# Optimization experiments

Measured on AMD Instinct MI355X. Metric: run time of the kernel, lower is better.

## Reference

```python
import jax, jax.numpy as jnp
import numpy as np

T, D, I, E, G, LG, K = 2048, 1024, 512, 32, 8, 4, 6
SI = 2 * I  # shared expert inter dim = n_shared_experts * inter_dim
ROUTE_SCALE = 1.0


def setup_inputs() -> dict:
    key = jax.random.key(0)
    ks = jax.random.split(key, 16)
    s = 0.02
    f = jnp.float32
    return {
        "x": jax.random.normal(ks[0], (T, D), f),
        "router_w": jax.random.normal(ks[1], (E, D), f) * s,
        "router_b": jax.random.normal(ks[2], (E,), f) * s,
        "W1": jax.random.normal(ks[3], (E, D, I), f) * s,
        "b1": jax.random.normal(ks[4], (E, I), f) * s,
        "W2": jax.random.normal(ks[5], (E, D, I), f) * s,
        "b2": jax.random.normal(ks[6], (E, I), f) * s,
        "W3": jax.random.normal(ks[7], (E, I, D), f) * s,
        "b3": jax.random.normal(ks[8], (E, D), f) * s,
        "sw1": jax.random.normal(ks[9], (D, SI), f) * s,
        "sb1": jax.random.normal(ks[10], (SI,), f) * s,
        "sw2": jax.random.normal(ks[11], (D, SI), f) * s,
        "sb2": jax.random.normal(ks[12], (SI,), f) * s,
        "sw3": jax.random.normal(ks[13], (SI, D), f) * s,
        "sb3": jax.random.normal(ks[14], (D,), f) * s,
    }


def _route(x, router_w, router_b):
    # Router: softmax scores (fp32), group-limited top-k.
    logits = x @ router_w.T + router_b                      # [T, E]
    scores = jax.nn.softmax(logits.astype(jnp.float32), axis=-1)
    original = scores
    sg = scores.reshape(x.shape[0], G, E // G)              # [T, G, E/G]
    # no router bias -> group score = sum of top-2 expert scores per group
    group_scores = jnp.sum(jax.lax.top_k(sg, 2)[0], axis=-1)  # [T, G]
    _, gidx = jax.lax.top_k(group_scores, LG)               # [T, LG]
    keep = jnp.zeros((x.shape[0], G), bool).at[jnp.arange(x.shape[0])[:, None], gidx].set(True)
    masked = jnp.where(keep[:, :, None], sg, -jnp.inf).reshape(x.shape[0], E)
    _, idx = jax.lax.top_k(masked, K)                       # [T, K]
    vals = jnp.take_along_axis(original, idx, axis=1) * ROUTE_SCALE
    return vals.astype(x.dtype), idx


def reference(x, router_w, router_b, W1, b1, W2, b2, W3, b3, sw1, sb1, sw2, sb2, sw3, sb3):
    vals, idx = _route(x, router_w, router_b)
    # dense gate matrix [T, E]; top-k indices per row are distinct
    gates = jnp.zeros((x.shape[0], E), x.dtype).at[jnp.arange(x.shape[0])[:, None], idx].set(vals)
    # routed experts: Expert(x) = W3 @ silu(w1(x) * w2(x))
    h1 = jnp.einsum('td,edi->tei', x, W1) + b1              # [T, E, I]
    h2 = jnp.einsum('td,edi->tei', x, W2) + b2
    h = jax.nn.silu(h1 * h2)
    y = jnp.einsum('tei,eid->td', h * gates[:, :, None], W3) + gates @ b3
    # shared expert
    z = jax.nn.silu((x @ sw1 + sb1) * (x @ sw2 + sb2)) @ sw3 + sb3
    return y + z
```

## Files before the change

kernel.cpp:

```cpp
#include <hip/hip_runtime.h>
#include <hip/hip_bf16.h>
#include <math.h>

#define T_CONST 2048
#define D_CONST 1024
#define I_CONST 512
#define SI_CONST 1024
#define E_CONST 32
#define G_CONST 8
#define LG_CONST 4
#define KSEL 6
#define BK 32

typedef __attribute__((ext_vector_type(8))) short short8;
typedef __attribute__((ext_vector_type(4))) float floatx4;

__device__ inline unsigned pack_bf16(float a, float b) {
  __hip_bfloat162 h = __float22bfloat162_rn(float2{a, b});
  return *reinterpret_cast<unsigned*>(&h);
}

__device__ inline void gload16(const void* g, void* l) {
  __builtin_amdgcn_global_load_lds(
      (const __attribute__((address_space(1))) unsigned int*)g,
      (__attribute__((address_space(3))) unsigned int*)l, 16, 0, 0);
}

__global__ __launch_bounds__(256) void cvt_x(const float* __restrict__ in,
                                             __hip_bfloat16* __restrict__ out) {
  size_t i = ((size_t)blockIdx.x * 256 + threadIdx.x) * 4;
  float4 v = *(const float4*)&in[i];
  uint2 u{pack_bf16(v.x, v.y), pack_bf16(v.z, v.w)};
  *(uint2*)&out[i] = u;
}

__global__ __launch_bounds__(256) void cvt_rwt(const float* __restrict__ rw,
                                               float* __restrict__ rwt) {
  int i = blockIdx.x * 256 + threadIdx.x;
  int d = i >> 5, e = i & 31;
  rwt[d * 32 + e] = rw[e * D_CONST + d];
}

__global__ __launch_bounds__(256) void transpose_all(
    const float* __restrict__ W1, const float* __restrict__ W2,
    const float* __restrict__ W3, const float* __restrict__ sw1,
    const float* __restrict__ sw2, const float* __restrict__ sw3,
    __hip_bfloat16* __restrict__ W1t, __hip_bfloat16* __restrict__ W2t,
    __hip_bfloat16* __restrict__ W3t, __hip_bfloat16* __restrict__ sw1t,
    __hip_bfloat16* __restrict__ sw2t, __hip_bfloat16* __restrict__ sw3t) {
  __shared__ float tile[64][65];
  int b = blockIdx.x;
  const float* in;
  __hip_bfloat16* out;
  int K, N, k0, n0;
  if (b < 8192) {
    int local = b & 4095;
    int mat = local >> 7, rem = local & 127;
    K = 1024; N = 512;
    in = ((b < 4096) ? W1 : W2) + (size_t)mat * (1024 * 512);
    out = ((b < 4096) ? W1t : W2t) + (size_t)mat * (1024 * 512);
    n0 = (rem & 7) * 64; k0 = (rem >> 3) * 64;
  } else if (b < 12288) {
    int local = b - 8192;
    int mat = local >> 7, rem = local & 127;
    K = 512; N = 1024;
    in = W3 + (size_t)mat * (512 * 1024);
    out = W3t + (size_t)mat * (512 * 1024);
    n0 = (rem & 15) * 64; k0 = (rem >> 4) * 64;
  } else {
    int local = b - 12288;
    int which = local >> 8, rem = local & 255;
    K = 1024; N = 1024;
    in = which == 0 ? sw1 : which == 1 ? sw2 : sw3;
    out = which == 0 ? sw1t : which == 1 ? sw2t : sw3t;
    n0 = (rem & 15) * 64; k0 = (rem >> 4) * 64;
  }
  int tid = threadIdx.x;
  int tr = tid >> 4, tc4 = (tid & 15) * 4;
#pragma unroll
  for (int i = 0; i < 4; ++i) {
    float4 v = *(const float4*)&in[(size_t)(k0 + tr + 16 * i) * N + n0 + tc4];
    tile[tr + 16 * i][tc4 + 0] = v.x;
    tile[tr + 16 * i][tc4 + 1] = v.y;
    tile[tr + 16 * i][tc4 + 2] = v.z;
    tile[tr + 16 * i][tc4 + 3] = v.w;
  }
  __syncthreads();
#pragma unroll
  for (int i = 0; i < 4; ++i) {
    int n = tr + 16 * i;
    unsigned lo = pack_bf16(tile[tc4 + 0][n], tile[tc4 + 1][n]);
    unsigned hi = pack_bf16(tile[tc4 + 2][n], tile[tc4 + 3][n]);
    uint2 u{lo, hi};
    *(uint2*)&out[(size_t)(n0 + n) * K + k0 + tc4] = u;
  }
}

__global__ __launch_bounds__(256) void router2(
    const float* __restrict__ x, const float* __restrict__ rwt,
    const float* __restrict__ rb, int* __restrict__ counts,
    int* __restrict__ stok, float* __restrict__ gatel) {
  const int lane = threadIdx.x & 63;
  const int wv = threadIdx.x >> 6;
  const int t = blockIdx.x * 4 + wv;
  const int e = lane & 31, h = lane >> 5;
  const float* xp = x + (size_t)t * D_CONST;
  float s = 0.f;
#pragma unroll 8
  for (int d = h; d < D_CONST; d += 2) s = fmaf(xp[d], rwt[d * 32 + e], s);
  s += __shfl_xor(s, 32);
  s += rb[e];
  float mx = s;
#pragma unroll
  for (int m = 16; m >= 1; m >>= 1) mx = fmaxf(mx, __shfl_xor(mx, m));
  float p = expf(s - mx);
  float sum = p;
#pragma unroll
  for (int m = 16; m >= 1; m >>= 1) sum += __shfl_xor(sum, m);
  float sc = p / sum;
  float a = sc, bb = __shfl_xor(a, 1);
  float hi = fmaxf(a, bb), lo = fminf(a, bb);
  float oh = __shfl_xor(hi, 2), ol = __shfl_xor(lo, 2);
  float gs = fmaxf(fmaxf(hi + oh, hi + lo), oh + ol);
  const int g = e >> 2;
  unsigned keep = 0;
  float gv = gs;
#pragma unroll
  for (int r = 0; r < LG_CONST; ++r) {
    float v = gv;
    int gi = g;
#pragma unroll
    for (int m = 16; m >= 1; m >>= 1) {
      float ov = __shfl_xor(v, m);
      int og = __shfl_xor(gi, m);
      if (ov > v || (ov == v && og < gi)) { v = ov; gi = og; }
    }
    keep |= 1u << gi;
    if (g == gi) gv = -1e30f;
  }
  float cand = ((keep >> g) & 1u) ? sc : -1e30f;
  int sel_e = -1;
  float sel_v = 0.f;
#pragma unroll
  for (int r = 0; r < KSEL; ++r) {
    float v = cand;
    int ei = e;
#pragma unroll
    for (int m = 16; m >= 1; m >>= 1) {
      float ov = __shfl_xor(v, m);
      int oe = __shfl_xor(ei, m);
      if (ov > v || (ov == v && oe < ei)) { v = ov; ei = oe; }
    }
    if (lane == r) { sel_e = ei; sel_v = v; }
    if (e == ei) cand = -1e30f;
  }
  if (lane < KSEL) {
    int pos = atomicAdd(&counts[sel_e], 1);
    stok[sel_e * T_CONST + pos] = t;
    gatel[sel_e * T_CONST + pos] = sel_v;
  }
}

__global__ __launch_bounds__(64) void plan_build(
    const int* __restrict__ counts, int* __restrict__ offsets,
    int* __restrict__ plan_up, int* __restrict__ plan_dn, int* __restrict__ meta) {
  const int lane = threadIdx.x;
  for (int i = lane; i < 128; i += 64) {
    int ent = (E_CONST << 8) | i;
    plan_up[i] = ent;
    plan_dn[i] = ent;
  }
  int cnt = (lane < E_CONST) ? counts[lane] : 0;
  int incl = cnt;
#pragma unroll
  for (int d = 1; d < 64; d <<= 1) {
    int v = __shfl_up(incl, d);
    if (lane >= d) incl += v;
  }
  if (lane < E_CONST) offsets[lane] = incl - cnt;
  if (lane == E_CONST - 1) offsets[E_CONST] = incl;
  int mbs = (cnt + 127) >> 7;
  int pm = mbs;
#pragma unroll
  for (int d = 1; d < 64; d <<= 1) {
    int v = __shfl_up(pm, d);
    if (lane >= d) pm += v;
  }
  int pmex = pm - mbs;
  if (lane < E_CONST) {
    int ub = 128 + pmex * 4, db = 128 + pmex * 8;
    for (int mb = 0; mb < mbs; ++mb) {
#pragma unroll
      for (int nb = 0; nb < 4; ++nb)
        plan_up[ub + mb * 4 + nb] = (lane << 8) | (mb << 3) | nb;
#pragma unroll
      for (int nb = 0; nb < 8; ++nb)
        plan_dn[db + mb * 8 + nb] = (lane << 8) | (mb << 3) | nb;
    }
  }
  if (lane == E_CONST - 1) {
    meta[0] = 128 + pm * 4;
    meta[1] = 128 + pm * 8;
  }
}

__global__ __launch_bounds__(256) void gather_x(
    const __hip_bfloat16* __restrict__ xbf, const int* __restrict__ counts,
    const int* __restrict__ offsets, const int* __restrict__ stok,
    const float* __restrict__ gatel, __hip_bfloat16* __restrict__ Xg,
    float* __restrict__ cgate, int* __restrict__ tcnt, int* __restrict__ tslot) {
  int e = blockIdx.x;
  int cnt = counts[e];
  int row = blockIdx.y * 16 + (threadIdx.x >> 4);
  if (row >= cnt) return;
  int seg = threadIdx.x & 15;
  int tok = stok[e * T_CONST + row];
  int dst = offsets[e] + row;
  const uint4* src = (const uint4*)(xbf + (size_t)tok * D_CONST);
  uint4* d = (uint4*)(Xg + (size_t)dst * D_CONST);
#pragma unroll
  for (int i = 0; i < 8; ++i) d[i * 16 + seg] = src[i * 16 + seg];
  if (seg == 0) {
    cgate[dst] = gatel[e * T_CONST + row];
    int sl = atomicAdd(&tcnt[tok], 1);
    tslot[tok * 8 + sl] = dst;
  }
}

__global__ __launch_bounds__(256, 2) void up_fused(
    const __hip_bfloat16* __restrict__ Xg, const __hip_bfloat16* __restrict__ xbf,
    const __hip_bfloat16* __restrict__ W1t, const __hip_bfloat16* __restrict__ W2t,
    const __hip_bfloat16* __restrict__ sw1t, const __hip_bfloat16* __restrict__ sw2t,
    const float* __restrict__ b1, const float* __restrict__ b2,
    const float* __restrict__ sb1, const float* __restrict__ sb2,
    const int* __restrict__ counts, const int* __restrict__ offsets,
    const int* __restrict__ plan, const int* __restrict__ meta,
    __hip_bfloat16* __restrict__ He, __hip_bfloat16* __restrict__ Hs) {
  if ((int)blockIdx.x >= meta[0]) return;
  const int ent = plan[blockIdx.x];
  const int z = ent >> 8;
  const int m0 = ((ent >> 3) & 31) * 128;
  const int n0 = (ent & 7) * 128;
  const bool SH = (z == E_CONST);
  const int cnt = SH ? T_CONST : counts[z];
  const int base = SH ? 0 : offsets[z];

  const __hip_bfloat16* Ab = SH ? (xbf + (size_t)m0 * D_CONST)
                                : (Xg + (size_t)(base + m0) * D_CONST);
  const __hip_bfloat16* B1 = SH ? (sw1t + (size_t)n0 * D_CONST)
                                : (W1t + ((size_t)z * I_CONST + n0) * D_CONST);
  const __hip_bfloat16* B2 = SH ? (sw2t + (size_t)n0 * D_CONST)
                                : (W2t + ((size_t)z * I_CONST + n0) * D_CONST);

  __shared__ short As[2 * 4096], Bs1[2 * 4096], Bs2[2 * 4096];

  const int tid = threadIdx.x, lane = tid & 63, wv = tid >> 6;
  const int l15 = lane & 15, quad = lane >> 4;
  const int wm = wv & 1, wn = wv >> 1;
  const int lr = lane >> 2;
  const int lc = lane & 3;

  const __hip_bfloat16 *aG[2], *b1G[2], *b2G[2];
#pragma unroll
  for (int i = 0; i < 2; ++i) {
    int r = wv * 32 + i * 16 + lr;
    int kap = lc ^ ((r >> 1) & 3);
    aG[i]  = Ab + (size_t)r * D_CONST + kap * 8;
    b1G[i] = B1 + (size_t)r * D_CONST + kap * 8;
    b2G[i] = B2 + (size_t)r * D_CONST + kap * 8;
  }
  const int ldsu = wv * 1024 + lane * 8;

  floatx4 acc1[4][4] = {};
  floatx4 acc2[4][4] = {};

  const int nIter = D_CONST / BK;

  auto stage = [&](int slot, int kk) {
    const int sb = slot * 4096;
#pragma unroll
    for (int i = 0; i < 2; ++i) {
      gload16(aG[i] + kk,  &As [sb + ldsu + i * 512]);
      gload16(b1G[i] + kk, &Bs1[sb + ldsu + i * 512]);
      gload16(b2G[i] + kk, &Bs2[sb + ldsu + i * 512]);
    }
  };

  stage(0, 0);
  int cur = 0;

  for (int s = 0; s < nIter; ++s) {
    int kn = (s + 1 < nIter) ? (s + 1) * BK : s * BK;
    stage(cur ^ 1, kn);
    asm volatile("s_waitcnt vmcnt(6)" ::: "memory");
    __builtin_amdgcn_s_barrier();
    const int sb = cur * 4096;
    short8 a[4], x1[4], x2[4];
#pragma unroll
    for (int mi = 0; mi < 4; ++mi) {
      int m = wm * 64 + mi * 16 + l15;
      a[mi] = *(const short8*)&As[sb + m * 32 + (quad ^ ((m >> 1) & 3)) * 8];
    }
#pragma unroll
    for (int ni = 0; ni < 4; ++ni) {
      int n = wn * 64 + ni * 16 + l15;
      int u = sb + n * 32 + (quad ^ ((n >> 1) & 3)) * 8;
      x1[ni] = *(const short8*)&Bs1[u];
      x2[ni] = *(const short8*)&Bs2[u];
    }
    __builtin_amdgcn_s_setprio(1);
#pragma unroll
    for (int mi = 0; mi < 4; ++mi)
#pragma unroll
      for (int ni = 0; ni < 4; ++ni) {
        acc1[mi][ni] = __builtin_amdgcn_mfma_f32_16x16x32_bf16(a[mi], x1[ni], acc1[mi][ni], 0, 0, 0);
        acc2[mi][ni] = __builtin_amdgcn_mfma_f32_16x16x32_bf16(a[mi], x2[ni], acc2[mi][ni], 0, 0, 0);
      }
    __builtin_amdgcn_s_setprio(0);
    __builtin_amdgcn_s_barrier();
    cur ^= 1;
  }
  asm volatile("s_waitcnt vmcnt(0)" ::: "memory");

  const float* pb1 = SH ? sb1 : (b1 + (size_t)z * I_CONST);
  const float* pb2 = SH ? sb2 : (b2 + (size_t)z * I_CONST);
  __hip_bfloat16* outp = SH ? (Hs + (size_t)m0 * SI_CONST + n0)
                            : (He + (size_t)(base + m0) * I_CONST + n0);
  const int ldo = SH ? SI_CONST : I_CONST;
  float c1[4], c2[4];
#pragma unroll
  for (int ni = 0; ni < 4; ++ni) {
    int n = wn * 64 + ni * 16 + l15;
    c1[ni] = pb1[n0 + n];
    c2[ni] = pb2[n0 + n];
  }
#pragma unroll
  for (int mi = 0; mi < 4; ++mi) {
#pragma unroll
    for (int reg = 0; reg < 4; ++reg) {
      int m = wm * 64 + mi * 16 + quad * 4 + reg;
      if (m0 + m >= cnt) continue;
#pragma unroll
      for (int ni = 0; ni < 4; ++ni) {
        int n = wn * 64 + ni * 16 + l15;
        float h1 = acc1[mi][ni][reg] + c1[ni];
        float h2 = acc2[mi][ni][reg] + c2[ni];
        float p = h1 * h2;
        float s = p / (1.f + expf(-p));
        outp[(size_t)m * ldo + n] = __float2bfloat16(s);
      }
    }
  }
}

__global__ __launch_bounds__(256, 3) void down_fused(
    const __hip_bfloat16* __restrict__ He, const __hip_bfloat16* __restrict__ Hs,
    const __hip_bfloat16* __restrict__ W3t, const __hip_bfloat16* __restrict__ sw3t,
    const float* __restrict__ b3, const float* __restrict__ sb3,
    const int* __restrict__ counts, const int* __restrict__ offsets,
    const float* __restrict__ cgate, const int* __restrict__ plan,
    const int* __restrict__ meta, float* __restrict__ Yp, float* __restrict__ out) {
  if ((int)blockIdx.x >= meta[1]) return;
  const int ent = plan[blockIdx.x];
  const int z = ent >> 8;
  const int m0 = ((ent >> 3) & 31) * 128;
  const int n0 = (ent & 7) * 128;
  const bool SH = (z == E_CONST);
  const int cnt = SH ? T_CONST : counts[z];
  const int base = SH ? 0 : offsets[z];
  const int Kd = SH ? SI_CONST : I_CONST;

  const __hip_bfloat16* Ab = SH ? (Hs + (size_t)m0 * SI_CONST)
                                : (He + (size_t)(base + m0) * I_CONST);
  const __hip_bfloat16* Bb = SH ? (sw3t + (size_t)n0 * SI_CONST)
                                : (W3t + ((size_t)z * D_CONST + n0) * I_CONST);

  __shared__ short As[2 * 4096], Bs[2 * 4096];

  const int tid = threadIdx.x, lane = tid & 63, wv = tid >> 6;
  const int l15 = lane & 15, quad = lane >> 4;
  const int wm = wv & 1, wn = wv >> 1;
  const int lr = lane >> 2, lc = lane & 3;

  const __hip_bfloat16 *aG[2], *bG[2];
#pragma unroll
  for (int i = 0; i < 2; ++i) {
    int r = wv * 32 + i * 16 + lr;
    int kap = lc ^ ((r >> 1) & 3);
    aG[i] = Ab + (size_t)r * Kd + kap * 8;
    bG[i] = Bb + (size_t)r * Kd + kap * 8;
  }
  const int ldsu = wv * 1024 + lane * 8;

  floatx4 acc[4][4] = {};
  const int nIter = Kd / BK;

  auto stage = [&](int slot, int kk) {
    const int sb = slot * 4096;
#pragma unroll
    for (int i = 0; i < 2; ++i) {
      gload16(aG[i] + kk, &As[sb + ldsu + i * 512]);
      gload16(bG[i] + kk, &Bs[sb + ldsu + i * 512]);
    }
  };

  stage(0, 0);
  int cur = 0;

  for (int s = 0; s < nIter; ++s) {
    int kn = (s + 1 < nIter) ? (s + 1) * BK : s * BK;
    stage(cur ^ 1, kn);
    asm volatile("s_waitcnt vmcnt(4)" ::: "memory");
    __builtin_amdgcn_s_barrier();
    const int sb = cur * 4096;
    short8 a[4], bbf[4];
#pragma unroll
    for (int mi = 0; mi < 4; ++mi) {
      int m = wm * 64 + mi * 16 + l15;
      a[mi] = *(const short8*)&As[sb + m * 32 + (quad ^ ((m >> 1) & 3)) * 8];
    }
#pragma unroll
    for (int ni = 0; ni < 4; ++ni) {
      int n = wn * 64 + ni * 16 + l15;
      bbf[ni] = *(const short8*)&Bs[sb + n * 32 + (quad ^ ((n >> 1) & 3)) * 8];
    }
    __builtin_amdgcn_s_setprio(1);
#pragma unroll
    for (int mi = 0; mi < 4; ++mi)
#pragma unroll
      for (int ni = 0; ni < 4; ++ni)
        acc[mi][ni] = __builtin_amdgcn_mfma_f32_16x16x32_bf16(a[mi], bbf[ni], acc[mi][ni], 0, 0, 0);
    __builtin_amdgcn_s_setprio(0);
    __builtin_amdgcn_s_barrier();
    cur ^= 1;
  }
  asm volatile("s_waitcnt vmcnt(0)" ::: "memory");

  float bias[4];
#pragma unroll
  for (int ni = 0; ni < 4; ++ni) {
    int n = n0 + wn * 64 + ni * 16 + l15;
    bias[ni] = SH ? sb3[n] : b3[(size_t)z * D_CONST + n];
  }
#pragma unroll
  for (int mi = 0; mi < 4; ++mi) {
#pragma unroll
    for (int reg = 0; reg < 4; ++reg) {
      int m = wm * 64 + mi * 16 + quad * 4 + reg;
      if (m0 + m >= cnt) continue;
#pragma unroll
      for (int ni = 0; ni < 4; ++ni) {
        int n = n0 + wn * 64 + ni * 16 + l15;
        float v = acc[mi][ni][reg] + bias[ni];
        if (SH) {
          out[(size_t)(m0 + m) * D_CONST + n] = v;
        } else {
          int grow = base + m0 + m;
          Yp[(size_t)grow * D_CONST + n] = cgate[grow] * v;
        }
      }
    }
  }
}

__global__ __launch_bounds__(256) void combine(
    const float* __restrict__ Yp, const int* __restrict__ tslot,
    float* __restrict__ out) {
  const int t = blockIdx.x;
  const int d = threadIdx.x * 4;
  const int* ts = &tslot[t * 8];
  float4 o = *(const float4*)&out[(size_t)t * D_CONST + d];
#pragma unroll
  for (int k = 0; k < KSEL; ++k) {
    float4 y = *(const float4*)&Yp[(size_t)ts[k] * D_CONST + d];
    o.x += y.x; o.y += y.y; o.z += y.z; o.w += y.w;
  }
  *(float4*)&out[(size_t)t * D_CONST + d] = o;
}

extern "C" void kernel_launch(void* const* d_in, const int* in_sizes, int n_in,
                              void* d_out, int out_size, void* d_ws, size_t ws_size,
                              hipStream_t stream) {
  const float* x   = (const float*)d_in[0];
  const float* rw  = (const float*)d_in[1];
  const float* rb  = (const float*)d_in[2];
  const float* W1  = (const float*)d_in[3];
  const float* b1  = (const float*)d_in[4];
  const float* W2  = (const float*)d_in[5];
  const float* b2  = (const float*)d_in[6];
  const float* W3  = (const float*)d_in[7];
  const float* b3  = (const float*)d_in[8];
  const float* sw1 = (const float*)d_in[9];
  const float* sb1 = (const float*)d_in[10];
  const float* sw2 = (const float*)d_in[11];
  const float* sb2 = (const float*)d_in[12];
  const float* sw3 = (const float*)d_in[13];
  const float* sb3 = (const float*)d_in[14];
  float* out = (float*)d_out;

  char* w = (char*)d_ws;
  size_t off = 0;
  auto alloc = [&](size_t bytes) {
    char* p = w + off;
    off += (bytes + 255) & ~(size_t)255;
    return p;
  };
  int* counts = (int*)alloc(E_CONST * 4);
  int* offsets = (int*)alloc((E_CONST + 1) * 4);
  int* meta = (int*)alloc(16);
  int* plan_up = (int*)alloc(768 * 4);
  int* plan_dn = (int*)alloc(1280 * 4);
  int* tcnt = (int*)alloc((size_t)T_CONST * 4);
  int* tslot = (int*)alloc((size_t)T_CONST * 8 * 4);
  int* stok = (int*)alloc((size_t)E_CONST * T_CONST * 4);
  float* gatel = (float*)alloc((size_t)E_CONST * T_CONST * 4);
  float* rwt = (float*)alloc((size_t)D_CONST * E_CONST * 4);
  float* cgate = (float*)alloc((size_t)T_CONST * KSEL * 4);
  __hip_bfloat16* x_bf = (__hip_bfloat16*)alloc((size_t)T_CONST * D_CONST * 2);
  __hip_bfloat16* Xg = (__hip_bfloat16*)alloc((size_t)(T_CONST * KSEL + 128) * D_CONST * 2);
  __hip_bfloat16* W1t = (__hip_bfloat16*)alloc((size_t)E_CONST * D_CONST * I_CONST * 2);
  __hip_bfloat16* W2t = (__hip_bfloat16*)alloc((size_t)E_CONST * D_CONST * I_CONST * 2);
  __hip_bfloat16* W3t = (__hip_bfloat16*)alloc((size_t)E_CONST * I_CONST * D_CONST * 2);
  __hip_bfloat16* sw1t = (__hip_bfloat16*)alloc((size_t)D_CONST * SI_CONST * 2);
  __hip_bfloat16* sw2t = (__hip_bfloat16*)alloc((size_t)D_CONST * SI_CONST * 2);
  __hip_bfloat16* sw3t = (__hip_bfloat16*)alloc((size_t)SI_CONST * D_CONST * 2);
  __hip_bfloat16* He = (__hip_bfloat16*)alloc((size_t)(T_CONST * KSEL + 128) * I_CONST * 2);
  __hip_bfloat16* Hs = (__hip_bfloat16*)alloc((size_t)T_CONST * SI_CONST * 2);
  float* Yp = (float*)W1t;

  hipMemsetAsync(counts, 0, E_CONST * sizeof(int), stream);
  hipMemsetAsync(tcnt, 0, (size_t)T_CONST * sizeof(int), stream);
  cvt_rwt<<<(D_CONST * E_CONST) / 256, 256, 0, stream>>>(rw, rwt);
  cvt_x<<<(T_CONST * D_CONST) / 1024, 256, 0, stream>>>(x, x_bf);
  transpose_all<<<13056, 256, 0, stream>>>(W1, W2, W3, sw1, sw2, sw3,
                                           W1t, W2t, W3t, sw1t, sw2t, sw3t);
  router2<<<T_CONST / 4, 256, 0, stream>>>(x, rwt, rb, counts, stok, gatel);
  plan_build<<<1, 64, 0, stream>>>(counts, offsets, plan_up, plan_dn, meta);
  gather_x<<<dim3(E_CONST, T_CONST / 16), 256, 0, stream>>>(
      x_bf, counts, offsets, stok, gatel, Xg, cgate, tcnt, tslot);
  up_fused<<<768, 256, 0, stream>>>(
      Xg, x_bf, W1t, W2t, sw1t, sw2t, b1, b2, sb1, sb2, counts, offsets,
      plan_up, meta, He, Hs);
  down_fused<<<1280, 256, 0, stream>>>(
      He, Hs, W3t, sw3t, b3, sb3, counts, offsets, cgate, plan_dn, meta, Yp, out);
  combine<<<T_CONST, 256, 0, stream>>>(Yp, tslot, out);
}
```

Baseline: 461.1 us.

## Triple-buffer GEMM K-loop, remap up-GEMM block order, rewrite weight transpose via bf16 LDS

Both the up and down grouped GEMMs move from double to triple buffering of LDS tiles. Loads are now issued two K-steps ahead with adjusted vmcnt waits, so more memory latency is hidden. The up kernel remaps block index to plan entries in 8 contiguous chunks, likely to improve locality across XCDs. The weight transpose kernel now packs bf16 before the LDS write and uses an XOR-swizzled bf16 tile with 16-byte stores. Extra LDS per block may reduce occupancy, especially in down_fused, which requests 3 blocks per CU.

Result: slower. 473.6 us (+2.7%).

```diff
diff --git a/kernel.cpp b/kernel.cpp
--- a/kernel.cpp
+++ b/kernel.cpp
@@ -48,7 +48,7 @@
     __hip_bfloat16* __restrict__ W1t, __hip_bfloat16* __restrict__ W2t,
     __hip_bfloat16* __restrict__ W3t, __hip_bfloat16* __restrict__ sw1t,
     __hip_bfloat16* __restrict__ sw2t, __hip_bfloat16* __restrict__ sw3t) {
-  __shared__ float tile[64][65];
+  __shared__ short tile[64 * 64];
   int b = blockIdx.x;
   const float* in;
   __hip_bfloat16* out;
@@ -75,24 +75,29 @@
     out = which == 0 ? sw1t : which == 1 ? sw2t : sw3t;
     n0 = (rem & 15) * 64; k0 = (rem >> 4) * 64;
   }
-  int tid = threadIdx.x;
-  int tr = tid >> 4, tc4 = (tid & 15) * 4;
-#pragma unroll
-  for (int i = 0; i < 4; ++i) {
-    float4 v = *(const float4*)&in[(size_t)(k0 + tr + 16 * i) * N + n0 + tc4];
-    tile[tr + 16 * i][tc4 + 0] = v.x;
-    tile[tr + 16 * i][tc4 + 1] = v.y;
-    tile[tr + 16 * i][tc4 + 2] = v.z;
-    tile[tr + 16 * i][tc4 + 3] = v.w;
+  const int tid = threadIdx.x;
+  const int u = tid & 15, tr = tid >> 4;
+  float4 v[4];
+#pragma unroll
+  for (int r = 0; r < 4; ++r)
+    v[r] = *(const float4*)&in[(size_t)(k0 + 4 * tr + r) * N + n0 + 4 * u];
+#pragma unroll
+  for (int j = 0; j < 4; ++j) {
+    int n = 4 * u + j;
+    unsigned lo = pack_bf16(((const float*)&v[0])[j], ((const float*)&v[1])[j]);
+    unsigned hi = pack_bf16(((const float*)&v[2])[j], ((const float*)&v[3])[j]);
+    int cu = (tr >> 1) ^ (u & 7);
+    int off = n * 64 + cu * 8 + (tr & 1) * 4;
+    *(uint2*)&tile[off] = uint2{lo, hi};
   }
   __syncthreads();
 #pragma unroll
-  for (int i = 0; i < 4; ++i) {
-    int n = tr + 16 * i;
-    unsigned lo = pack_bf16(tile[tc4 + 0][n], tile[tc4 + 1][n]);
-    unsigned hi = pack_bf16(tile[tc4 + 2][n], tile[tc4 + 3][n]);
-    uint2 u{lo, hi};
-    *(uint2*)&out[(size_t)(n0 + n) * K + k0 + tc4] = u;
+  for (int s2 = 0; s2 < 2; ++s2) {
+    int id = tid + s2 * 256;
+    int n = id >> 3, cu = id & 7;
+    int cx = cu ^ ((n >> 2) & 7);
+    uint4 o = *(const uint4*)&tile[n * 64 + cx * 8];
+    *(uint4*)&out[(size_t)(n0 + n) * K + k0 + cu * 8] = o;
   }
 }
 
@@ -236,8 +241,12 @@
     const int* __restrict__ counts, const int* __restrict__ offsets,
     const int* __restrict__ plan, const int* __restrict__ meta,
     __hip_bfloat16* __restrict__ He, __hip_bfloat16* __restrict__ Hs) {
-  if ((int)blockIdx.x >= meta[0]) return;
-  const int ent = plan[blockIdx.x];
+  const int nw = meta[0];
+  const int bx = blockIdx.x;
+  if (bx >= nw) return;
+  const int q = nw >> 3, r = nw & 7, c = bx & 7, sl = bx >> 3;
+  const int j = (c < r ? c * (q + 1) : r * (q + 1) + (c - r) * q) + sl;
+  const int ent = plan[j];
   const int z = ent >> 8;
   const int m0 = ((ent >> 3) & 31) * 128;
   const int n0 = (ent & 7) * 128;
@@ -252,7 +261,7 @@
   const __hip_bfloat16* B2 = SH ? (sw2t + (size_t)n0 * D_CONST)
                                 : (W2t + ((size_t)z * I_CONST + n0) * D_CONST);
 
-  __shared__ short As[2 * 4096], Bs1[2 * 4096], Bs2[2 * 4096];
+  __shared__ short As[3 * 4096], Bs1[3 * 4096], Bs2[3 * 4096];
 
   const int tid = threadIdx.x, lane = tid & 63, wv = tid >> 6;
   const int l15 = lane & 15, quad = lane >> 4;
@@ -263,11 +272,11 @@
   const __hip_bfloat16 *aG[2], *b1G[2], *b2G[2];
 #pragma unroll
   for (int i = 0; i < 2; ++i) {
-    int r = wv * 32 + i * 16 + lr;
-    int kap = lc ^ ((r >> 1) & 3);
-    aG[i]  = Ab + (size_t)r * D_CONST + kap * 8;
-    b1G[i] = B1 + (size_t)r * D_CONST + kap * 8;
-    b2G[i] = B2 + (size_t)r * D_CONST + kap * 8;
+    int rr = wv * 32 + i * 16 + lr;
+    int kap = lc ^ ((rr >> 1) & 3);
+    aG[i]  = Ab + (size_t)rr * D_CONST + kap * 8;
+    b1G[i] = B1 + (size_t)rr * D_CONST + kap * 8;
+    b2G[i] = B2 + (size_t)rr * D_CONST + kap * 8;
   }
   const int ldsu = wv * 1024 + lane * 8;
 
@@ -287,14 +296,15 @@
   };
 
   stage(0, 0);
-  int cur = 0;
+  stage(1, BK);
+  int sl0 = 0, sl1 = 1, sl2 = 2;
 
   for (int s = 0; s < nIter; ++s) {
-    int kn = (s + 1 < nIter) ? (s + 1) * BK : s * BK;
-    stage(cur ^ 1, kn);
-    asm volatile("s_waitcnt vmcnt(6)" ::: "memory");
+    int kn = (s + 2 < nIter) ? (s + 2) * BK : (nIter - 1) * BK;
+    stage(sl2, kn);
+    asm volatile("s_waitcnt vmcnt(12)" ::: "memory");
     __builtin_amdgcn_s_barrier();
-    const int sb = cur * 4096;
+    const int sb = sl0 * 4096;
     short8 a[4], x1[4], x2[4];
 #pragma unroll
     for (int mi = 0; mi < 4; ++mi) {
@@ -304,9 +314,9 @@
 #pragma unroll
     for (int ni = 0; ni < 4; ++ni) {
       int n = wn * 64 + ni * 16 + l15;
-      int u = sb + n * 32 + (quad ^ ((n >> 1) & 3)) * 8;
-      x1[ni] = *(const short8*)&Bs1[u];
-      x2[ni] = *(const short8*)&Bs2[u];
+      int uo = sb + n * 32 + (quad ^ ((n >> 1) & 3)) * 8;
+      x1[ni] = *(const short8*)&Bs1[uo];
+      x2[ni] = *(const short8*)&Bs2[uo];
     }
     __builtin_amdgcn_s_setprio(1);
 #pragma unroll
@@ -318,7 +328,7 @@
       }
     __builtin_amdgcn_s_setprio(0);
     __builtin_amdgcn_s_barrier();
-    cur ^= 1;
+    int t = sl0; sl0 = sl1; sl1 = sl2; sl2 = t;
   }
   asm volatile("s_waitcnt vmcnt(0)" ::: "memory");
 
@@ -346,8 +356,8 @@
         float h1 = acc1[mi][ni][reg] + c1[ni];
         float h2 = acc2[mi][ni][reg] + c2[ni];
         float p = h1 * h2;
-        float s = p / (1.f + expf(-p));
-        outp[(size_t)m * ldo + n] = __float2bfloat16(s);
+        float sg = p / (1.f + expf(-p));
+        outp[(size_t)m * ldo + n] = __float2bfloat16(sg);
       }
     }
   }
@@ -375,7 +385,7 @@
   const __hip_bfloat16* Bb = SH ? (sw3t + (size_t)n0 * SI_CONST)
                                 : (W3t + ((size_t)z * D_CONST + n0) * I_CONST);
 
-  __shared__ short As[2 * 4096], Bs[2 * 4096];
+  __shared__ short As[3 * 4096], Bs[3 * 4096];
 
   const int tid = threadIdx.x, lane = tid & 63, wv = tid >> 6;
   const int l15 = lane & 15, quad = lane >> 4;
@@ -385,10 +395,10 @@
   const __hip_bfloat16 *aG[2], *bG[2];
 #pragma unroll
   for (int i = 0; i < 2; ++i) {
-    int r = wv * 32 + i * 16 + lr;
-    int kap = lc ^ ((r >> 1) & 3);
-    aG[i] = Ab + (size_t)r * Kd + kap * 8;
-    bG[i] = Bb + (size_t)r * Kd + kap * 8;
+    int rr = wv * 32 + i * 16 + lr;
+    int kap = lc ^ ((rr >> 1) & 3);
+    aG[i] = Ab + (size_t)rr * Kd + kap * 8;
+    bG[i] = Bb + (size_t)rr * Kd + kap * 8;
   }
   const int ldsu = wv * 1024 + lane * 8;
 
@@ -405,14 +415,15 @@
   };
 
   stage(0, 0);
-  int cur = 0;
+  stage(1, BK);
+  int sl0 = 0, sl1 = 1, sl2 = 2;
 
   for (int s = 0; s < nIter; ++s) {
-    int kn = (s + 1 < nIter) ? (s + 1) * BK : s * BK;
-    stage(cur ^ 1, kn);
-    asm volatile("s_waitcnt vmcnt(4)" ::: "memory");
+    int kn = (s + 2 < nIter) ? (s + 2) * BK : (nIter - 1) * BK;
+    stage(sl2, kn);
+    asm volatile("s_waitcnt vmcnt(8)" ::: "memory");
     __builtin_amdgcn_s_barrier();
-    const int sb = cur * 4096;
+    const int sb = sl0 * 4096;
     short8 a[4], bbf[4];
 #pragma unroll
     for (int mi = 0; mi < 4; ++mi) {
@@ -432,7 +443,7 @@
         acc[mi][ni] = __builtin_amdgcn_mfma_f32_16x16x32_bf16(a[mi], bbf[ni], acc[mi][ni], 0, 0, 0);
     __builtin_amdgcn_s_setprio(0);
     __builtin_amdgcn_s_barrier();
-    cur ^= 1;
+    int t = sl0; sl0 = sl1; sl1 = sl2; sl2 = t;
   }
   asm volatile("s_waitcnt vmcnt(0)" ::: "memory");
 
```
